# Kernel tuning notes

Measured on AMD Instinct MI355X. Metric: run time of the kernel, lower is better.

Reference implementation:

```python
import jax, jax.numpy as jnp
import numpy as np

B, N, M = 8, 4096, 4096

def _sqdist(x, y):
    # x: [B,N,3], y: [B,M,3] -> squared euclidean distances [B,N,M]
    return jnp.sum((x[:, :, None, :] - y[:, None, :, :]) ** 2, axis=-1)

def _approx_match(xyz1, xyz2):
    # Faithful port of Fan et al. approxmatch.cu (used by PyTorchEMD's
    # earth_mover_distance): annealed soft-assignment over 10 levels.
    b, n, _ = xyz1.shape
    m = xyz2.shape[1]
    d2 = _sqdist(xyz1, xyz2)                      # [B,N,M]
    factorl = max(n, m) / n
    factorr = max(n, m) / m
    satl = jnp.full((b, n), factorl, d2.dtype)    # remaining mass, left
    satr = jnp.full((b, m), factorr, d2.dtype)    # remaining mass, right
    match = jnp.zeros_like(d2)
    # levels: -4^7 .. -4^-1, then 0 (exactly as in approxmatch.cu)
    levels = [-(4.0 ** j) for j in range(7, -2, -1)] + [0.0]
    for level in levels:
        w = jnp.exp(level * d2) * satr[:, None, :]                 # [B,N,M]
        w = w * (satl / (jnp.sum(w, axis=2) + 1e-9))[:, :, None]   # row normalize
        ss2 = jnp.sum(w, axis=1)                                   # [B,M]
        ratio = jnp.minimum(satr / (ss2 + 1e-9), 1.0)
        w = w * ratio[:, None, :]                                  # col capacity clamp
        match = match + w
        satl = jnp.maximum(satl - jnp.sum(w, axis=2), 0.0)
        satr = jnp.maximum(satr - ss2 * ratio, 0.0)
    return match, d2

def setup_inputs() -> dict:
    key = jax.random.key(0)
    k1, k2 = jax.random.split(key)
    array1 = jax.random.uniform(k1, (B, N, 3), dtype=jnp.float32)
    array2 = jax.random.uniform(k2, (B, M, 3), dtype=jnp.float32)
    return {"array1": array1, "array2": array2}

def reference(array1, array2):
    match, d2 = _approx_match(array1, array2)
    dist = jnp.sum(match * d2, axis=(1, 2))   # per-batch EMD (squared-dist transport cost), [B]
    return jnp.mean(dist) / array1.shape[1]
```

## Files before the change

kernel.cpp:

```cpp
#include <hip/hip_runtime.h>


#define BB 8
#define NN 4096
#define MM 4096

constexpr int BLK   = 256;
constexpr int S     = 16;
constexpr int R     = 4;
constexpr int RPB   = (BLK / S) * R;
constexpr int CHUNK = 2048;
constexpr int G     = (CHUNK / S) / 4;

#if defined(__has_builtin)
#if __has_builtin(__builtin_amdgcn_exp2f)
#define EXP2F(x) __builtin_amdgcn_exp2f(x)
#endif
#if __has_builtin(__builtin_amdgcn_logf)
#define LOG2F(x) __builtin_amdgcn_logf(x)
#endif
#endif
#ifndef EXP2F
#define EXP2F(x) exp2f(x)
#endif
#ifndef LOG2F
#define LOG2F(x) log2f(x)
#endif

__global__ void emd_init(float* __restrict__ satl, float* __restrict__ satr,
                         float* __restrict__ bsum, float* __restrict__ slsum,
                         float* __restrict__ scal, float* __restrict__ out) {
    int i = blockIdx.x * blockDim.x + threadIdx.x;
    if (i < BB * NN) satl[i] = 1.0f;
    if (i < BB * MM) satr[i] = 1.0f;
    if (i < BB)      bsum[i] = 0.0f;
    if (i < BB)      slsum[i] = 0.0f;
    if (i < BB * 5)  scal[i] = 0.0f;
    if (i == 0)      out[0]  = 0.0f;
}

#define A_LOAD(vv, gg)                                           \
    _Pragma("unroll")                                            \
    for (int k = 0; k < 4; ++k) vv[k] = q[((gg)*4 + k)*S + s];

#define A_COMP(vv)                                               \
    _Pragma("unroll")                                            \
    for (int k = 0; k < 4; ++k) {                                \
        float4 v = vv[k];                                        \
        _Pragma("unroll")                                        \
        for (int r = 0; r < R; ++r) {                            \
            float dot = fmaf(z1[r], v.z, fmaf(y1[r], v.y, x1[r]*v.x)); \
            float arg = fmaf(m2c, dot, v.w + cpp[r]);            \
            acc[r] += EXP2F(arg);                                \
        }                                                        \
    }

__global__ __launch_bounds__(BLK, 2) void emd_passA(
        const float* __restrict__ xyz1, const float* __restrict__ xyz2,
        const float* __restrict__ satl, const float* __restrict__ satr,
        float* __restrict__ sl, float c) {
    __shared__ float4 q[CHUNK];
    const int b    = blockIdx.x / (NN / RPB);
    const int tile = blockIdx.x % (NN / RPB);
    const float* x2b = xyz2 + (size_t)b * MM * 3;
    const float* srb = satr + (size_t)b * MM;

    const int g = threadIdx.x / S, s = threadIdx.x % S;
    const int n0 = tile * RPB + g * R;
    const float* p = xyz1 + ((size_t)b * NN + n0) * 3;
    const float m2c = -2.0f * c;
    float x1[R], y1[R], z1[R], cpp[R], acc[R];
    #pragma unroll
    for (int r = 0; r < R; ++r) {
        x1[r] = p[3*r]; y1[r] = p[3*r+1]; z1[r] = p[3*r+2];
        cpp[r] = c * (x1[r]*x1[r] + y1[r]*y1[r] + z1[r]*z1[r]);
        acc[r] = 0.0f;
    }

    for (int c0 = 0; c0 < MM; c0 += CHUNK) {
        __syncthreads();
        for (int m = threadIdx.x; m < CHUNK; m += BLK) {
            int mm = c0 + m;
            float xx = x2b[3*mm], yy = x2b[3*mm+1], zz = x2b[3*mm+2];
            float qq = xx*xx + yy*yy + zz*zz;
            q[m] = make_float4(xx, yy, zz, fmaf(c, qq, LOG2F(srb[mm])));
        }
        __syncthreads();
        float4 va[4], vb[4];
        A_LOAD(va, 0);
        #pragma unroll 1
        for (int gs = 0; gs < G; gs += 2) {
            A_LOAD(vb, gs + 1);
            A_COMP(va);
            if (gs + 2 < G) { A_LOAD(va, gs + 2); }
            A_COMP(vb);
        }
    }
    #pragma unroll
    for (int r = 0; r < R; ++r) {
        acc[r] += __shfl_xor(acc[r], 1);
        acc[r] += __shfl_xor(acc[r], 2);
        acc[r] += __shfl_xor(acc[r], 4);
        acc[r] += __shfl_xor(acc[r], 8);
    }
    if (s == 0) {
        #pragma unroll
        for (int r = 0; r < R; ++r) {
            int gi = b * NN + n0 + r;
            sl[gi] = satl[gi] / (acc[r] + 1e-9f);
        }
    }
}

__global__ __launch_bounds__(BLK, 2) void emd_passB(
        const float* __restrict__ xyz1, const float* __restrict__ xyz2,
        const float* __restrict__ sl, float* __restrict__ satr,
        float* __restrict__ sr2, float* __restrict__ bsum,
        int do_sum, float c) {
    __shared__ float4 q[CHUNK];
    const int b    = blockIdx.x / (MM / RPB);
    const int tile = blockIdx.x % (MM / RPB);
    const float* x1b = xyz1 + (size_t)b * NN * 3;
    const float* slb = sl + (size_t)b * NN;

    const int g = threadIdx.x / S, s = threadIdx.x % S;
    const int m0 = tile * RPB + g * R;
    const float* qp = xyz2 + ((size_t)b * MM + m0) * 3;
    const float m2c = -2.0f * c;
    float x1[R], y1[R], z1[R], cpp[R], acc[R];
    #pragma unroll
    for (int r = 0; r < R; ++r) {
        x1[r] = qp[3*r]; y1[r] = qp[3*r+1]; z1[r] = qp[3*r+2];
        cpp[r] = c * (x1[r]*x1[r] + y1[r]*y1[r] + z1[r]*z1[r]);
        acc[r] = 0.0f;
    }

    for (int c0 = 0; c0 < NN; c0 += CHUNK) {
        __syncthreads();
        for (int n = threadIdx.x; n < CHUNK; n += BLK) {
            int nn = c0 + n;
            float xx = x1b[3*nn], yy = x1b[3*nn+1], zz = x1b[3*nn+2];
            float pp = xx*xx + yy*yy + zz*zz;
            q[n] = make_float4(xx, yy, zz, fmaf(c, pp, LOG2F(slb[nn])));
        }
        __syncthreads();
        float4 va[4], vb[4];
        A_LOAD(va, 0);
        #pragma unroll 1
        for (int gs = 0; gs < G; gs += 2) {
            A_LOAD(vb, gs + 1);
            A_COMP(va);
            if (gs + 2 < G) { A_LOAD(va, gs + 2); }
            A_COMP(vb);
        }
    }
    #pragma unroll
    for (int r = 0; r < R; ++r) {
        acc[r] += __shfl_xor(acc[r], 1);
        acc[r] += __shfl_xor(acc[r], 2);
        acc[r] += __shfl_xor(acc[r], 4);
        acc[r] += __shfl_xor(acc[r], 8);
    }
    float part = 0.0f;
    if (s == 0) {
        #pragma unroll
        for (int r = 0; r < R; ++r) {
            int gi = b * MM + m0 + r;
            float sr    = satr[gi];
            float ss2   = acc[r] * sr;
            float ratio = fminf(sr / (ss2 + 1e-9f), 1.0f);
            float sn    = fmaxf(sr - ss2 * ratio, 0.0f);
            sr2[gi]  = sr * ratio;
            satr[gi] = sn;
            part += sn;
        }
    }
    if (do_sum) {
        part += __shfl_xor(part, 1);
        part += __shfl_xor(part, 2);
        part += __shfl_xor(part, 4);
        part += __shfl_xor(part, 8);
        part += __shfl_xor(part, 16);
        part += __shfl_xor(part, 32);
        if ((threadIdx.x & 63) == 0) atomicAdd(&bsum[b], part);
    }
}

#define CA0_LOAD(vv, ww, gg)                                     \
    _Pragma("unroll")                                            \
    for (int k = 0; k < 4; ++k) {                                \
        int idx = ((gg)*4 + k)*S + s;                            \
        vv[k] = q[idx]; ww[k] = w[idx];                          \
    }

#define CA0_COMP(vv, ww)                                         \
    _Pragma("unroll")                                            \
    for (int k = 0; k < 4; ++k) {                                \
        float4 v = vv[k]; float2 wv = ww[k];                     \
        _Pragma("unroll")                                        \
        for (int r = 0; r < R; ++r) {                            \
            float dot = fmaf(z1[r], v.z, fmaf(y1[r], v.y, x1[r]*v.x)); \
            float arg = fmaf(m2cn, dot, v.w + cnpp[r]);          \
            float en  = EXP2F(arg);                              \
            acc2[r] = fmaf(en, wv.y, acc2[r]);                   \
            float e2 = en * en;                                  \
            float t  = (e2 * e2) * wv.x;                         \
            rd[r]   += t;                                        \
            costA[r] = fmaf(t, arg, costA[r]);                   \
        }                                                        \
    }

__global__ __launch_bounds__(BLK, 2) void emd_passCA0(
        const float* __restrict__ xyz1, const float* __restrict__ xyz2,
        float* __restrict__ sl, float* __restrict__ satl,
        const float* __restrict__ sr2, const float* __restrict__ satr_next,
        float* __restrict__ out, float cl, float cn) {
    __shared__ float4 q[CHUNK];
    __shared__ float2 w[CHUNK];
    const int b    = blockIdx.x / (NN / RPB);
    const int tile = blockIdx.x % (NN / RPB);
    const float* x2b = xyz2 + (size_t)b * MM * 3;
    const float* s2b = sr2 + (size_t)b * MM;
    const float* srb = satr_next + (size_t)b * MM;

    const int g = threadIdx.x / S, s = threadIdx.x % S;
    const int n0 = tile * RPB + g * R;
    const float* pp_ = xyz1 + ((size_t)b * NN + n0) * 3;
    const float m2cn = -2.0f * cn;
    const float icn  = 1.0f / cn;
    float x1[R], y1[R], z1[R], cnpp[R], rd[R], costA[R], acc2[R], slv[R];
    #pragma unroll
    for (int r = 0; r < R; ++r) {
        x1[r] = pp_[3*r]; y1[r] = pp_[3*r+1]; z1[r] = pp_[3*r+2];
        cnpp[r] = cn * (x1[r]*x1[r] + y1[r]*y1[r] + z1[r]*z1[r]);
        rd[r] = 0.0f; costA[r] = 0.0f; acc2[r] = 0.0f;
        slv[r] = sl[b * NN + n0 + r];
    }

    for (int c0 = 0; c0 < MM; c0 += CHUNK) {
        __syncthreads();
        for (int m = threadIdx.x; m < CHUNK; m += BLK) {
            int mm = c0 + m;
            float xx = x2b[3*mm], yy = x2b[3*mm+1], zz = x2b[3*mm+2];
            float qq = xx*xx + yy*yy + zz*zz;
            q[m] = make_float4(xx, yy, zz, cn * qq);
            w[m] = make_float2(s2b[mm], srb[mm]);
        }
        __syncthreads();

        float4 va[4], vb[4]; float2 wa[4], wb[4];
        CA0_LOAD(va, wa, 0);
        #pragma unroll 1
        for (int gs = 0; gs < G; gs += 2) {
            CA0_LOAD(vb, wb, gs + 1);
            CA0_COMP(va, wa);
            if (gs + 2 < G) { CA0_LOAD(va, wa, gs + 2); }
            CA0_COMP(vb, wb);
        }
    }

    #pragma unroll
    for (int r = 0; r < R; ++r) {
        rd[r] += __shfl_xor(rd[r], 1);
        rd[r] += __shfl_xor(rd[r], 2);
        rd[r] += __shfl_xor(rd[r], 4);
        rd[r] += __shfl_xor(rd[r], 8);
        acc2[r] += __shfl_xor(acc2[r], 1);
        acc2[r] += __shfl_xor(acc2[r], 2);
        acc2[r] += __shfl_xor(acc2[r], 4);
        acc2[r] += __shfl_xor(acc2[r], 8);
    }

    float csum = 0.0f;
    #pragma unroll
    for (int r = 0; r < R; ++r) csum += (costA[r] * icn) * slv[r];
    csum += __shfl_xor(csum, 1);
    csum += __shfl_xor(csum, 2);
    csum += __shfl_xor(csum, 4);
    csum += __shfl_xor(csum, 8);
    csum += __shfl_xor(csum, 16);
    csum += __shfl_xor(csum, 32);
    if ((threadIdx.x & 63) == 0)
        atomicAdd(out, csum * (1.0f / (float)(BB * NN)));

    if (s == 0) {
        #pragma unroll
        for (int r = 0; r < R; ++r) {
            int gi = b * NN + n0 + r;
            float sa = fmaxf(satl[gi] - rd[r] * slv[r], 0.0f);
            satl[gi] = sa;
            sl[gi] = sa / (acc2[r] + 1e-9f);
        }
    }
}

#define CA1_LOAD(vv, aa, gg)                                     \
    _Pragma("unroll")                                            \
    for (int k = 0; k < 4; ++k) {                                \
        int idx = ((gg)*4 + k)*S + s;                            \
        vv[k] = q[idx]; aa[k] = qa[idx];                         \
    }

#define CA1_COMP(vv, aa)                                         \
    _Pragma("unroll")                                            \
    for (int k = 0; k < 4; ++k) {                                \
        float4 v = vv[k]; float qq = aa[k];                      \
        _Pragma("unroll")                                        \
        for (int r = 0; r < R; ++r) {                            \
            float dot = fmaf(z1[r], v.z, fmaf(y1[r], v.y, x1[r]*v.x)); \
            float t   = EXP2F(fmaf(m2cl, dot, v.w + clpp[r]));   \
            rd[r] += t;                                          \
            float d2 = fmaf(-2.0f, dot, pp[r]) + qq;             \
            cost[r] = fmaf(t, d2, cost[r]);                      \
        }                                                        \
    }

__global__ __launch_bounds__(BLK, 2) void emd_passCA1(
        const float* __restrict__ xyz1, const float* __restrict__ xyz2,
        float* __restrict__ sl, float* __restrict__ satl,
        const float* __restrict__ sr2, const float* __restrict__ bsum,
        float* __restrict__ slsum, float* __restrict__ out, float cl) {
    __shared__ float4 q[CHUNK];
    __shared__ float  qa[CHUNK];
    const int b    = blockIdx.x / (NN / RPB);
    const int tile = blockIdx.x % (NN / RPB);
    const float* x2b = xyz2 + (size_t)b * MM * 3;
    const float* s2b = sr2 + (size_t)b * MM;

    const int g = threadIdx.x / S, s = threadIdx.x % S;
    const int n0 = tile * RPB + g * R;
    const float* pp_ = xyz1 + ((size_t)b * NN + n0) * 3;
    const float m2cl = -2.0f * cl;
    float x1[R], y1[R], z1[R], pp[R], clpp[R], rd[R], cost[R], slv[R];
    #pragma unroll
    for (int r = 0; r < R; ++r) {
        x1[r] = pp_[3*r]; y1[r] = pp_[3*r+1]; z1[r] = pp_[3*r+2];
        pp[r]   = x1[r]*x1[r] + y1[r]*y1[r] + z1[r]*z1[r];
        clpp[r] = cl * pp[r];
        rd[r] = 0.0f; cost[r] = 0.0f;
        slv[r] = sl[b * NN + n0 + r];
    }

    for (int c0 = 0; c0 < MM; c0 += CHUNK) {
        __syncthreads();
        for (int m = threadIdx.x; m < CHUNK; m += BLK) {
            int mm = c0 + m;
            float xx = x2b[3*mm], yy = x2b[3*mm+1], zz = x2b[3*mm+2];
            float qq = xx*xx + yy*yy + zz*zz;
            q[m]  = make_float4(xx, yy, zz, fmaf(cl, qq, LOG2F(s2b[mm])));
            qa[m] = qq;
        }
        __syncthreads();

        float4 va[4], vb[4]; float aa[4], ab[4];
        CA1_LOAD(va, aa, 0);
        #pragma unroll 1
        for (int gs = 0; gs < G; gs += 2) {
            CA1_LOAD(vb, ab, gs + 1);
            CA1_COMP(va, aa);
            if (gs + 2 < G) { CA1_LOAD(va, aa, gs + 2); }
            CA1_COMP(vb, ab);
        }
    }

    #pragma unroll
    for (int r = 0; r < R; ++r) {
        rd[r] += __shfl_xor(rd[r], 1);
        rd[r] += __shfl_xor(rd[r], 2);
        rd[r] += __shfl_xor(rd[r], 4);
        rd[r] += __shfl_xor(rd[r], 8);
    }

    float csum = 0.0f;
    #pragma unroll
    for (int r = 0; r < R; ++r) csum += cost[r] * slv[r];
    csum += __shfl_xor(csum, 1);
    csum += __shfl_xor(csum, 2);
    csum += __shfl_xor(csum, 4);
    csum += __shfl_xor(csum, 8);
    csum += __shfl_xor(csum, 16);
    csum += __shfl_xor(csum, 32);
    if ((threadIdx.x & 63) == 0)
        atomicAdd(out, csum * (1.0f / (float)(BB * NN)));

    float part = 0.0f;
    if (s == 0) {
        float bs = bsum[b];
        #pragma unroll
        for (int r = 0; r < R; ++r) {
            int gi = b * NN + n0 + r;
            float sa = fmaxf(satl[gi] - rd[r] * slv[r], 0.0f);
            satl[gi] = sa;
            float s9 = sa / (bs + 1e-9f);
            sl[gi] = s9;
            part += s9;
        }
    }
    part += __shfl_xor(part, 1);
    part += __shfl_xor(part, 2);
    part += __shfl_xor(part, 4);
    part += __shfl_xor(part, 8);
    part += __shfl_xor(part, 16);
    part += __shfl_xor(part, 32);
    if ((threadIdx.x & 63) == 0) atomicAdd(&slsum[b], part);
}

__global__ void emd_lvl9_col(const float* __restrict__ xyz2,
                             const float* __restrict__ satr,
                             const float* __restrict__ slsum,
                             float* __restrict__ scal) {
    int i = blockIdx.x * blockDim.x + threadIdx.x;
    int b = i / MM;
    const float* qp = xyz2 + (size_t)i * 3;
    float sr = satr[i];
    float ss2 = sr * slsum[b];
    float ratio = fminf(sr / (ss2 + 1e-9f), 1.0f);
    float s2 = sr * ratio;
    float x = qp[0], y = qp[1], z = qp[2];
    float v0 = s2, v1 = s2*x, v2 = s2*y, v3 = s2*z;
    float v4 = s2 * (x*x + y*y + z*z);
    #pragma unroll
    for (int d = 1; d < 64; d <<= 1) {
        v0 += __shfl_xor(v0, d); v1 += __shfl_xor(v1, d);
        v2 += __shfl_xor(v2, d); v3 += __shfl_xor(v3, d);
        v4 += __shfl_xor(v4, d);
    }
    if ((threadIdx.x & 63) == 0) {
        atomicAdd(&scal[b*5+0], v0); atomicAdd(&scal[b*5+1], v1);
        atomicAdd(&scal[b*5+2], v2); atomicAdd(&scal[b*5+3], v3);
        atomicAdd(&scal[b*5+4], v4);
    }
}

__global__ void emd_lvl9_cost(const float* __restrict__ xyz1,
                              const float* __restrict__ sl,
                              const float* __restrict__ scal,
                              float* __restrict__ out) {
    int i = blockIdx.x * blockDim.x + threadIdx.x;
    int b = i / NN;
    float W  = scal[b*5+0], Wx = scal[b*5+1], Wy = scal[b*5+2];
    float Wz = scal[b*5+3], Q  = scal[b*5+4];
    const float* p = xyz1 + (size_t)i * 3;
    float x = p[0], y = p[1], z = p[2];
    float pp = x*x + y*y + z*z;
    float dotw = x*Wx + y*Wy + z*Wz;
    float c = sl[i] * (pp * W + Q - 2.0f * dotw);
    #pragma unroll
    for (int d = 1; d < 64; d <<= 1) c += __shfl_xor(c, d);
    if ((threadIdx.x & 63) == 0)
        atomicAdd(out, c * (1.0f / (float)(BB * NN)));
}

extern "C" void kernel_launch(void* const* d_in, const int* in_sizes, int n_in,
                              void* d_out, int out_size, void* d_ws, size_t ws_size,
                              hipStream_t stream) {
    const float* xyz1 = (const float*)d_in[0];
    const float* xyz2 = (const float*)d_in[1];
    float* out  = (float*)d_out;

    float* satl  = (float*)d_ws;
    float* sl    = satl  + BB * NN;
    float* satr  = sl    + BB * NN;
    float* sr2   = satr  + BB * MM;
    float* bsum  = sr2   + BB * MM;
    float* slsum = bsum  + BB;
    float* scal  = slsum + BB;

    emd_init<<<(BB * NN + 255) / 256, 256, 0, stream>>>(satl, satr, bsum,
                                                        slsum, scal, out);

    const double levels[10] = {-16384.0, -4096.0, -1024.0, -256.0, -64.0,
                               -16.0, -4.0, -1.0, -0.25, 0.0};
    const double LOG2E = 1.4426950408889634;
    float c[10];
    for (int l = 0; l < 10; ++l) c[l] = (float)(levels[l] * LOG2E);

    const int grid = BB * (NN / RPB);

    emd_passA<<<grid, BLK, 0, stream>>>(xyz1, xyz2, satl, satr, sl, c[0]);
    for (int l = 0; l <= 8; ++l) {
        emd_passB<<<grid, BLK, 0, stream>>>(xyz1, xyz2, sl, satr, sr2, bsum,
                                            (l == 8) ? 1 : 0, c[l]);
        if (l < 8)
            emd_passCA0<<<grid, BLK, 0, stream>>>(
                xyz1, xyz2, sl, satl, sr2, satr, out, c[l], c[l + 1]);
        else
            emd_passCA1<<<grid, BLK, 0, stream>>>(
                xyz1, xyz2, sl, satl, sr2, bsum, slsum, out, c[l]);
    }
    emd_lvl9_col<<<BB * MM / 256, 256, 0, stream>>>(xyz2, satr, slsum, scal);
    emd_lvl9_cost<<<BB * NN / 256, 256, 0, stream>>>(xyz1, sl, scal, out);
}
```

Measured before the change: 898.4 us.

## Fold scale into point coords, recover cost from exp argument, raise occupancy

The -2c scale is now folded into the per-row point coordinates, so the exponent argument is built with three FMAs and no separate dot product. The CA1 cost no longer computes d2 per pair. It accumulates t*arg and t*log2(w) and recovers the distance-weighted sum by algebra, with log2 clamped to avoid -inf. Rows per thread and the shared-memory chunk are halved and launch bounds raised to 4 blocks to increase occupancy. In exchange there is less register reuse per loaded point, and the recovered cost may lose precision through cancellation in (c1-c2)/cl.

```diff
diff --git a/kernel.cpp b/kernel.cpp
--- a/kernel.cpp
+++ b/kernel.cpp
@@ -7,9 +7,9 @@
 
 constexpr int BLK   = 256;
 constexpr int S     = 16;
-constexpr int R     = 4;
+constexpr int R     = 2;
 constexpr int RPB   = (BLK / S) * R;
-constexpr int CHUNK = 2048;
+constexpr int CHUNK = 1024;
 constexpr int G     = (CHUNK / S) / 4;
 
 #if defined(__has_builtin)
@@ -39,23 +39,25 @@
     if (i == 0)      out[0]  = 0.0f;
 }
 
-#define A_LOAD(vv, gg)                                           \
+#define AB_LOAD(vv, gg)                                          \
     _Pragma("unroll")                                            \
     for (int k = 0; k < 4; ++k) vv[k] = q[((gg)*4 + k)*S + s];
 
-#define A_COMP(vv)                                               \
+#define AB_COMP(vv)                                              \
     _Pragma("unroll")                                            \
     for (int k = 0; k < 4; ++k) {                                \
         float4 v = vv[k];                                        \
         _Pragma("unroll")                                        \
         for (int r = 0; r < R; ++r) {                            \
-            float dot = fmaf(z1[r], v.z, fmaf(y1[r], v.y, x1[r]*v.x)); \
-            float arg = fmaf(m2c, dot, v.w + cpp[r]);            \
+            float a0 = v.w + cpp[r];                             \
+            float a1 = fmaf(zs[r], v.z, a0);                     \
+            float a2 = fmaf(ys[r], v.y, a1);                     \
+            float arg = fmaf(xs[r], v.x, a2);                    \
             acc[r] += EXP2F(arg);                                \
         }                                                        \
     }
 
-__global__ __launch_bounds__(BLK, 2) void emd_passA(
+__global__ __launch_bounds__(BLK, 4) void emd_passA(
         const float* __restrict__ xyz1, const float* __restrict__ xyz2,
         const float* __restrict__ satl, const float* __restrict__ satr,
         float* __restrict__ sl, float c) {
@@ -69,11 +71,12 @@
     const int n0 = tile * RPB + g * R;
     const float* p = xyz1 + ((size_t)b * NN + n0) * 3;
     const float m2c = -2.0f * c;
-    float x1[R], y1[R], z1[R], cpp[R], acc[R];
-    #pragma unroll
-    for (int r = 0; r < R; ++r) {
-        x1[r] = p[3*r]; y1[r] = p[3*r+1]; z1[r] = p[3*r+2];
-        cpp[r] = c * (x1[r]*x1[r] + y1[r]*y1[r] + z1[r]*z1[r]);
+    float xs[R], ys[R], zs[R], cpp[R], acc[R];
+    #pragma unroll
+    for (int r = 0; r < R; ++r) {
+        float x = p[3*r], y = p[3*r+1], z = p[3*r+2];
+        cpp[r] = c * (x*x + y*y + z*z);
+        xs[r] = m2c * x; ys[r] = m2c * y; zs[r] = m2c * z;
         acc[r] = 0.0f;
     }
 
@@ -87,13 +90,13 @@
         }
         __syncthreads();
         float4 va[4], vb[4];
-        A_LOAD(va, 0);
+        AB_LOAD(va, 0);
         #pragma unroll 1
         for (int gs = 0; gs < G; gs += 2) {
-            A_LOAD(vb, gs + 1);
-            A_COMP(va);
-            if (gs + 2 < G) { A_LOAD(va, gs + 2); }
-            A_COMP(vb);
+            AB_LOAD(vb, gs + 1);
+            AB_COMP(va);
+            if (gs + 2 < G) { AB_LOAD(va, gs + 2); }
+            AB_COMP(vb);
         }
     }
     #pragma unroll
@@ -112,7 +115,7 @@
     }
 }
 
-__global__ __launch_bounds__(BLK, 2) void emd_passB(
+__global__ __launch_bounds__(BLK, 4) void emd_passB(
         const float* __restrict__ xyz1, const float* __restrict__ xyz2,
         const float* __restrict__ sl, float* __restrict__ satr,
         float* __restrict__ sr2, float* __restrict__ bsum,
@@ -127,11 +130,12 @@
     const int m0 = tile * RPB + g * R;
     const float* qp = xyz2 + ((size_t)b * MM + m0) * 3;
     const float m2c = -2.0f * c;
-    float x1[R], y1[R], z1[R], cpp[R], acc[R];
-    #pragma unroll
-    for (int r = 0; r < R; ++r) {
-        x1[r] = qp[3*r]; y1[r] = qp[3*r+1]; z1[r] = qp[3*r+2];
-        cpp[r] = c * (x1[r]*x1[r] + y1[r]*y1[r] + z1[r]*z1[r]);
+    float xs[R], ys[R], zs[R], cpp[R], acc[R];
+    #pragma unroll
+    for (int r = 0; r < R; ++r) {
+        float x = qp[3*r], y = qp[3*r+1], z = qp[3*r+2];
+        cpp[r] = c * (x*x + y*y + z*z);
+        xs[r] = m2c * x; ys[r] = m2c * y; zs[r] = m2c * z;
         acc[r] = 0.0f;
     }
 
@@ -145,13 +149,13 @@
         }
         __syncthreads();
         float4 va[4], vb[4];
-        A_LOAD(va, 0);
+        AB_LOAD(va, 0);
         #pragma unroll 1
         for (int gs = 0; gs < G; gs += 2) {
-            A_LOAD(vb, gs + 1);
-            A_COMP(va);
-            if (gs + 2 < G) { A_LOAD(va, gs + 2); }
-            A_COMP(vb);
+            AB_LOAD(vb, gs + 1);
+            AB_COMP(va);
+            if (gs + 2 < G) { AB_LOAD(va, gs + 2); }
+            AB_COMP(vb);
         }
     }
     #pragma unroll
@@ -199,8 +203,10 @@
         float4 v = vv[k]; float2 wv = ww[k];                     \
         _Pragma("unroll")                                        \
         for (int r = 0; r < R; ++r) {                            \
-            float dot = fmaf(z1[r], v.z, fmaf(y1[r], v.y, x1[r]*v.x)); \
-            float arg = fmaf(m2cn, dot, v.w + cnpp[r]);          \
+            float a0 = v.w + cnpp[r];                            \
+            float a1 = fmaf(zs[r], v.z, a0);                     \
+            float a2 = fmaf(ys[r], v.y, a1);                     \
+            float arg = fmaf(xs[r], v.x, a2);                    \
             float en  = EXP2F(arg);                              \
             acc2[r] = fmaf(en, wv.y, acc2[r]);                   \
             float e2 = en * en;                                  \
@@ -210,7 +216,7 @@
         }                                                        \
     }
 
-__global__ __launch_bounds__(BLK, 2) void emd_passCA0(
+__global__ __launch_bounds__(BLK, 4) void emd_passCA0(
         const float* __restrict__ xyz1, const float* __restrict__ xyz2,
         float* __restrict__ sl, float* __restrict__ satl,
         const float* __restrict__ sr2, const float* __restrict__ satr_next,
@@ -228,11 +234,12 @@
     const float* pp_ = xyz1 + ((size_t)b * NN + n0) * 3;
     const float m2cn = -2.0f * cn;
     const float icn  = 1.0f / cn;
-    float x1[R], y1[R], z1[R], cnpp[R], rd[R], costA[R], acc2[R], slv[R];
-    #pragma unroll
-    for (int r = 0; r < R; ++r) {
-        x1[r] = pp_[3*r]; y1[r] = pp_[3*r+1]; z1[r] = pp_[3*r+2];
-        cnpp[r] = cn * (x1[r]*x1[r] + y1[r]*y1[r] + z1[r]*z1[r]);
+    float xs[R], ys[R], zs[R], cnpp[R], rd[R], costA[R], acc2[R], slv[R];
+    #pragma unroll
+    for (int r = 0; r < R; ++r) {
+        float x = pp_[3*r], y = pp_[3*r+1], z = pp_[3*r+2];
+        cnpp[r] = cn * (x*x + y*y + z*z);
+        xs[r] = m2cn * x; ys[r] = m2cn * y; zs[r] = m2cn * z;
         rd[r] = 0.0f; costA[r] = 0.0f; acc2[r] = 0.0f;
         slv[r] = sl[b * NN + n0 + r];
     }
@@ -304,18 +311,21 @@
 #define CA1_COMP(vv, aa)                                         \
     _Pragma("unroll")                                            \
     for (int k = 0; k < 4; ++k) {                                \
-        float4 v = vv[k]; float qq = aa[k];                      \
+        float4 v = vv[k]; float lw = aa[k];                      \
         _Pragma("unroll")                                        \
         for (int r = 0; r < R; ++r) {                            \
-            float dot = fmaf(z1[r], v.z, fmaf(y1[r], v.y, x1[r]*v.x)); \
-            float t   = EXP2F(fmaf(m2cl, dot, v.w + clpp[r]));   \
+            float a0 = v.w + clpp[r];                            \
+            float a1 = fmaf(zs[r], v.z, a0);                     \
+            float a2 = fmaf(ys[r], v.y, a1);                     \
+            float arg = fmaf(xs[r], v.x, a2);                    \
+            float t   = EXP2F(arg);                              \
             rd[r] += t;                                          \
-            float d2 = fmaf(-2.0f, dot, pp[r]) + qq;             \
-            cost[r] = fmaf(t, d2, cost[r]);                      \
+            c1[r] = fmaf(t, arg, c1[r]);                         \
+            c2[r] = fmaf(t, lw, c2[r]);                          \
         }                                                        \
     }
 
-__global__ __launch_bounds__(BLK, 2) void emd_passCA1(
+__global__ __launch_bounds__(BLK, 4) void emd_passCA1(
         const float* __restrict__ xyz1, const float* __restrict__ xyz2,
         float* __restrict__ sl, float* __restrict__ satl,
         const float* __restrict__ sr2, const float* __restrict__ bsum,
@@ -331,13 +341,14 @@
     const int n0 = tile * RPB + g * R;
     const float* pp_ = xyz1 + ((size_t)b * NN + n0) * 3;
     const float m2cl = -2.0f * cl;
-    float x1[R], y1[R], z1[R], pp[R], clpp[R], rd[R], cost[R], slv[R];
-    #pragma unroll
-    for (int r = 0; r < R; ++r) {
-        x1[r] = pp_[3*r]; y1[r] = pp_[3*r+1]; z1[r] = pp_[3*r+2];
-        pp[r]   = x1[r]*x1[r] + y1[r]*y1[r] + z1[r]*z1[r];
-        clpp[r] = cl * pp[r];
-        rd[r] = 0.0f; cost[r] = 0.0f;
+    const float icl  = 1.0f / cl;
+    float xs[R], ys[R], zs[R], clpp[R], rd[R], c1[R], c2[R], slv[R];
+    #pragma unroll
+    for (int r = 0; r < R; ++r) {
+        float x = pp_[3*r], y = pp_[3*r+1], z = pp_[3*r+2];
+        clpp[r] = cl * (x*x + y*y + z*z);
+        xs[r] = m2cl * x; ys[r] = m2cl * y; zs[r] = m2cl * z;
+        rd[r] = 0.0f; c1[r] = 0.0f; c2[r] = 0.0f;
         slv[r] = sl[b * NN + n0 + r];
     }
 
@@ -347,8 +358,9 @@
             int mm = c0 + m;
             float xx = x2b[3*mm], yy = x2b[3*mm+1], zz = x2b[3*mm+2];
             float qq = xx*xx + yy*yy + zz*zz;
-            q[m]  = make_float4(xx, yy, zz, fmaf(cl, qq, LOG2F(s2b[mm])));
-            qa[m] = qq;
+            float lw = LOG2F(fmaxf(s2b[mm], 1e-30f));
+            q[m]  = make_float4(xx, yy, zz, fmaf(cl, qq, lw));
+            qa[m] = lw;
         }
         __syncthreads();
 
@@ -373,7 +385,7 @@
 
     float csum = 0.0f;
     #pragma unroll
-    for (int r = 0; r < R; ++r) csum += cost[r] * slv[r];
+    for (int r = 0; r < R; ++r) csum += ((c1[r] - c2[r]) * icl) * slv[r];
     csum += __shfl_xor(csum, 1);
     csum += __shfl_xor(csum, 2);
     csum += __shfl_xor(csum, 4);
```

New measurement: 1.024 ms. 1.14x slower.
